# Kernel optimization log

Hardware: AMD Instinct MI355X
Metric: run time of the kernel (lower is better)

## Reference

```python
import jax, jax.numpy as jnp
import numpy as np

N_NODES = 100000
N_EDGES = 1000000
N_GRAPHS = 512
IN_N, IN_E, HID, OUT = 32, 16, 64, 64
EPS = 0.1  # GINEConv eps buffer (not trainable)


def _mlp2(x, w0, b0, w1, b1):
    # 2-layer MLP: Linear -> ReLU -> Linear
    return jax.nn.relu(x @ w0 + b0) @ w1 + b1


def setup_inputs() -> dict:
    key = jax.random.key(0)
    ks = jax.random.split(key, 24)
    s = 0.05
    inp = {
        "x": jax.random.normal(ks[0], (N_NODES, IN_N), jnp.float32),
        "edge_index": jax.random.randint(ks[1], (2, N_EDGES), 0, N_NODES, jnp.int32),
        "edge_attr": jax.random.normal(ks[2], (N_EDGES, IN_E), jnp.float32),
        "batch": jnp.sort(jax.random.randint(ks[3], (N_NODES,), 0, N_GRAPHS, jnp.int32)),
        # node init MLP
        "wn0": jax.random.normal(ks[4], (IN_N, HID)) * s, "bn0": jnp.zeros((HID,)),
        "wn1": jax.random.normal(ks[5], (HID, HID)) * s, "bn1": jnp.zeros((HID,)),
        # edge init MLP
        "we0": jax.random.normal(ks[6], (IN_E, HID)) * s, "be0": jnp.zeros((HID,)),
        "we1": jax.random.normal(ks[7], (HID, HID)) * s, "be1": jnp.zeros((HID,)),
        # 3 residual GINE convs, MLP weights stacked on leading layer axis
        "cw0": jax.random.normal(ks[8], (3, HID, HID)) * s, "cb0": jnp.zeros((3, HID)),
        "cw1": jax.random.normal(ks[9], (3, HID, HID)) * s, "cb1": jnp.zeros((3, HID)),
        # final GINE conv MLP (hidden -> out)
        "lw0": jax.random.normal(ks[10], (HID, HID)) * s, "lb0": jnp.zeros((HID,)),
        "lw1": jax.random.normal(ks[11], (HID, OUT)) * s, "lb1": jnp.zeros((OUT,)),
    }
    return inp


def _gine_conv(x, src, dst, e, w0, b0, w1, b1):
    # message = relu(x_j + edge_attr); aggregate = scatter-add at target i
    msg = jax.nn.relu(x[src] + e)                       # [E, H]
    agg = jax.ops.segment_sum(msg, dst, num_segments=x.shape[0])  # [N, H]
    out = agg + (1.0 + EPS) * x
    return _mlp2(out, w0, b0, w1, b1)


def reference(x, edge_index, edge_attr, batch,
              wn0, bn0, wn1, bn1, we0, be0, we1, be1,
              cw0, cb0, cw1, cb1, lw0, lb0, lw1, lb1):
    src, dst = edge_index[0], edge_index[1]
    h = _mlp2(x, wn0, bn0, wn1, bn1)          # [N, HID]
    e = _mlp2(edge_attr, we0, be0, we1, be1)  # [E, HID]
    for l in range(3):  # residual GINE layers (BatchNorm never applied in source forward)
        h = jax.nn.relu(h + _gine_conv(h, src, dst, e, cw0[l], cb0[l], cw1[l], cb1[l]))
    h = _gine_conv(h, src, dst, e, lw0, lb0, lw1, lb1)  # [N, OUT]
    return jax.ops.segment_sum(h, batch, num_segments=N_GRAPHS)  # global_add_pool -> [G, OUT]
```

## Files before the change

### kernel.cpp

```cpp
#include <hip/hip_runtime.h>
#include <hip/hip_bf16.h>
#include <stdint.h>

#define N_NODES 100000
#define N_EDGES 1000000
#define N_GRAPHS 512
#define HID 64
#define INN 32
#define INE 16
#define CPAD 32

#define NPB 256
#define NBKT ((N_NODES + NPB - 1) / NPB)
#define BCAP 4096

#define S_NW0 0
#define S_NW1 4
#define S_EW0 12
#define S_EW1 16
#define S_CW0 24
#define S_CW1 48
#define S_LW0 72
#define S_LW1 80
#define NSLOT 88

typedef unsigned int uint32;
typedef unsigned short ushort16;
typedef __attribute__((ext_vector_type(8))) short bf8;
typedef __attribute__((ext_vector_type(4))) float f32x4;

__device__ __forceinline__ ushort16 f2bf(float f) {
    uint32 u = __float_as_uint(f);
    uint32 r = (u + 0x7fffu + ((u >> 16) & 1u)) >> 16;
    return (ushort16)r;
}
__device__ __forceinline__ uint32 pack_bf2(float lo, float hi) {
    return (uint32)f2bf(lo) | ((uint32)f2bf(hi) << 16);
}
__device__ __forceinline__ float bf_lo(uint32 v) { return __uint_as_float(v << 16); }
__device__ __forceinline__ float bf_hi(uint32 v) { return __uint_as_float(v & 0xffff0000u); }

__device__ __forceinline__ uint32 pack_h2(float lo, float hi) {
    union { _Float16 h[2]; uint32 u; } cv;
    cv.h[0] = (_Float16)lo; cv.h[1] = (_Float16)hi;
    return cv.u;
}
__device__ __forceinline__ float h2_lo(uint32 v) {
    union { uint32 u; _Float16 h[2]; } cv; cv.u = v; return (float)cv.h[0];
}
__device__ __forceinline__ float h2_hi(uint32 v) {
    union { uint32 u; _Float16 h[2]; } cv; cv.u = v; return (float)cv.h[1];
}
__device__ __forceinline__ uint32 pk_add_f16(uint32 a, uint32 b) {
    uint32 r; asm("v_pk_add_f16 %0, %1, %2" : "=v"(r) : "v"(a), "v"(b)); return r;
}
__device__ __forceinline__ uint32 pk_max_f16(uint32 a, uint32 b) {
    uint32 r; asm("v_pk_max_f16 %0, %1, %2" : "=v"(r) : "v"(a), "v"(b)); return r;
}


__global__ void k_diag(float* out, float val) { out[threadIdx.x] = val; }


__global__ __launch_bounds__(256) void k_prep(
    const float* __restrict__ wn0, const float* __restrict__ wn1,
    const float* __restrict__ we0, const float* __restrict__ we1,
    const float* __restrict__ cw0, const float* __restrict__ cw1,
    const float* __restrict__ lw0, const float* __restrict__ lw1,
    uint32* __restrict__ wfrag)
{
    for (int idx = threadIdx.x; idx < NSLOT * 64; idx += 256) {
        int s = idx >> 6, lane = idx & 63;
        const float* w; int K, NF, base;
        if (s < 4)       { w = wn0; K = 32; NF = 1; base = S_NW0; }
        else if (s < 12) { w = wn1; K = 64; NF = 2; base = S_NW1; }
        else if (s < 16) { w = we0; K = 16; NF = 1; base = S_EW0; }
        else if (s < 24) { w = we1; K = 64; NF = 2; base = S_EW1; }
        else if (s < 48) { int l = (s - S_CW0) >> 3; w = cw0 + l * 4096; K = 64; NF = 2; base = S_CW0 + l * 8; }
        else if (s < 72) { int l = (s - S_CW1) >> 3; w = cw1 + l * 4096; K = 64; NF = 2; base = S_CW1 + l * 8; }
        else if (s < 80) { w = lw0; K = 64; NF = 2; base = S_LW0; }
        else             { w = lw1; K = 64; NF = 2; base = S_LW1; }
        int r = s - base, t = r / NF, f = r - t * NF;
        int quad = lane >> 4, mn = lane & 15;
        uint32 out[4];
        #pragma unroll
        for (int p = 0; p < 4; p++) {
            int k0 = f * 32 + quad * 8 + p * 2;
            float lo = (k0 < K)     ? w[(size_t)k0 * HID + t * 16 + mn]       : 0.f;
            float hi = (k0 + 1 < K) ? w[(size_t)(k0 + 1) * HID + t * 16 + mn] : 0.f;
            out[p] = pack_bf2(lo, hi);
        }
        *(uint4*)(wfrag + (size_t)idx * 4) = make_uint4(out[0], out[1], out[2], out[3]);
    }
}


__global__ __launch_bounds__(256) void k_binA(const int* __restrict__ src,
                                              const int* __restrict__ dst,
                                              int* __restrict__ bcursor,
                                              uint2* __restrict__ binned) {
    __shared__ int cnt[NBKT];
    __shared__ int cur[NBKT];
    const int t = threadIdx.x;
    for (int b = t; b < NBKT; b += 256) cnt[b] = 0;
    __syncthreads();
    const int base = blockIdx.x * 4096;
    #pragma unroll
    for (int j = 0; j < 16; j++) {
        int e = base + j * 256 + t;
        if (e < N_EDGES) atomicAdd(&cnt[dst[e] >> 8], 1);
    }
    __syncthreads();
    for (int b = t; b < NBKT; b += 256) {
        int c = cnt[b];
        cur[b] = (c > 0) ? atomicAdd(&bcursor[(size_t)b * CPAD], c) : 0;
    }
    __syncthreads();
    #pragma unroll
    for (int j = 0; j < 16; j++) {
        int e = base + j * 256 + t;
        if (e < N_EDGES) {
            int d = dst[e];
            int bkt = d >> 8;
            int r = atomicAdd(&cur[bkt], 1);
            if (r < BCAP)
                binned[(size_t)bkt * BCAP + r] =
                    make_uint2((uint32)src[e] | ((uint32)(d & (NPB - 1)) << 17), (uint32)e);
        }
    }
}

__global__ __launch_bounds__(512) void k_scanB(const int* __restrict__ bcursor,
                                               int* __restrict__ bbase) {
    __shared__ int sh[512];
    const int t = threadIdx.x;
    int v = (t < NBKT) ? min(bcursor[(size_t)t * CPAD], BCAP) : 0;
    sh[t] = v; __syncthreads();
    for (int off = 1; off < 512; off <<= 1) {
        int u = (t >= off) ? sh[t - off] : 0;
        __syncthreads();
        sh[t] += u;
        __syncthreads();
    }
    if (t < NBKT) bbase[t] = sh[t] - v;
}

__global__ __launch_bounds__(256) void k_bucketB(const int* __restrict__ bcursor,
                                                 const int* __restrict__ bbase,
                                                 const uint2* __restrict__ binned,
                                                 int* __restrict__ rowptr,
                                                 int* __restrict__ perm_src,
                                                 int* __restrict__ eperm) {
    __shared__ int cnt[NPB];
    __shared__ int sh[NPB];
    const int b = blockIdx.x, t = threadIdx.x;
    const int n = min(bcursor[(size_t)b * CPAD], BCAP);
    const int base = bbase[b];
    const uint2* brec = binned + (size_t)b * BCAP;
    cnt[t] = 0;
    __syncthreads();
    for (int i = t; i < n; i += 256)
        atomicAdd(&cnt[brec[i].x >> 17], 1);
    __syncthreads();
    int c = cnt[t];
    sh[t] = c; __syncthreads();
    for (int off = 1; off < NPB; off <<= 1) {
        int u = (t >= off) ? sh[t - off] : 0;
        __syncthreads();
        sh[t] += u;
        __syncthreads();
    }
    int excl = sh[t] - c;
    int g = b * NPB + t;
    if (g < N_NODES) rowptr[g] = base + excl;
    if (b == 0 && t == 0) rowptr[N_NODES] = N_EDGES;
    cnt[t] = excl;
    __syncthreads();
    for (int i = t; i < n; i += 256) {
        uint2 r = brec[i];
        int dl = (int)(r.x >> 17);
        int p = base + atomicAdd(&cnt[dl], 1);
        perm_src[p] = (int)(r.x & 0x1FFFFu);
        eperm[p] = (int)r.y;
    }
}


template<int NF, bool RELU_RES, bool BF_IN>
__global__ __launch_bounds__(256, 4) void k_mlp_mfma(
    const void* __restrict__ in, const float* __restrict__ hprev, float* __restrict__ out,
    const uint32* __restrict__ wf0, const float* __restrict__ b0,
    const uint32* __restrict__ wf1, const float* __restrict__ b1,
    uint32* __restrict__ out_bf, int nrows)
{
    __shared__ ushort tile[4][16 * 72];
    const int wave = threadIdx.x >> 6, lane = threadIdx.x & 63;
    const int quad = lane >> 4, mn = lane & 15;
    ushort* T = &tile[wave][0];

    bf8 w0f[4][NF];
    #pragma unroll
    for (int t = 0; t < 4; t++)
        #pragma unroll
        for (int f = 0; f < NF; f++)
            w0f[t][f] = *(const bf8*)(wf0 + ((size_t)(t * NF + f) * 64 + lane) * 4);
    bf8 w1f[4][2];
    #pragma unroll
    for (int t = 0; t < 4; t++)
        #pragma unroll
        for (int f = 0; f < 2; f++)
            w1f[t][f] = *(const bf8*)(wf1 + ((size_t)(t * 2 + f) * 64 + lane) * 4);
    float b0v[4], b1v[4];
    #pragma unroll
    for (int t = 0; t < 4; t++) { b0v[t] = b0[t*16+mn]; b1v[t] = b1[t*16+mn]; }

    const int ebase = blockIdx.x * 64 + wave * 16;
    int rowA = ebase + mn; if (rowA > nrows - 1) rowA = nrows - 1;
    bf8 a1[NF];
    if (BF_IN) {
        const ushort* row = (const ushort*)in + (size_t)rowA * HID;
        #pragma unroll
        for (int f = 0; f < NF; f++)
            a1[f] = *(const bf8*)(row + f * 32 + quad * 8);
    } else {
        const float* inf = (const float*)in;
        #pragma unroll
        for (int f = 0; f < NF; f++) {
            const float4* pr = (const float4*)(inf + (size_t)rowA * (NF * 32) + f * 32 + quad * 8);
            float4 v0 = pr[0], v1 = pr[1];
            a1[f][0]=(short)f2bf(v0.x); a1[f][1]=(short)f2bf(v0.y);
            a1[f][2]=(short)f2bf(v0.z); a1[f][3]=(short)f2bf(v0.w);
            a1[f][4]=(short)f2bf(v1.x); a1[f][5]=(short)f2bf(v1.y);
            a1[f][6]=(short)f2bf(v1.z); a1[f][7]=(short)f2bf(v1.w);
        }
    }
    #pragma unroll
    for (int t = 0; t < 4; t++) {
        f32x4 c = {0.f, 0.f, 0.f, 0.f};
        #pragma unroll
        for (int f = 0; f < NF; f++)
            c = __builtin_amdgcn_mfma_f32_16x16x32_bf16(a1[f], w0f[t][f], c, 0, 0, 0);
        #pragma unroll
        for (int rg = 0; rg < 4; rg++) {
            int row = quad * 4 + rg;
            T[row * 72 + t * 16 + mn] = f2bf(fmaxf(c[rg] + b0v[t], 0.f));
        }
    }
    __builtin_amdgcn_wave_barrier();
    bf8 a2[2];
    #pragma unroll
    for (int f = 0; f < 2; f++)
        a2[f] = *(const bf8*)&T[mn * 72 + f * 32 + quad * 8];
    #pragma unroll
    for (int t = 0; t < 4; t++) {
        f32x4 c = {0.f, 0.f, 0.f, 0.f};
        c = __builtin_amdgcn_mfma_f32_16x16x32_bf16(a2[0], w1f[t][0], c, 0, 0, 0);
        c = __builtin_amdgcn_mfma_f32_16x16x32_bf16(a2[1], w1f[t][1], c, 0, 0, 0);
        #pragma unroll
        for (int rg = 0; rg < 4; rg++) {
            int row = quad * 4 + rg;
            int rowg = ebase + row;
            int rowc = (rowg < nrows) ? rowg : (nrows - 1);
            float v = c[rg] + b1v[t];
            if (RELU_RES) {
                float hv = hprev[(size_t)rowc * HID + t * 16 + mn];
                v = fmaxf(v + hv, 0.f);
            }
            if (rowg < nrows) out[(size_t)rowg * HID + t * 16 + mn] = v;
            T[row * 72 + t * 16 + mn] = f2bf(v);
        }
    }
    if (out_bf) {
        __builtin_amdgcn_wave_barrier();
        int half = lane >> 5, c32 = lane & 31;
        #pragma unroll
        for (int rr = 0; rr < 8; rr++) {
            int row = rr * 2 + half;
            int pos = ebase + row;
            if (pos < nrows) {
                uint32 w = *(const uint32*)&T[row * 72 + c32 * 2];
                out_bf[(size_t)pos * 32 + c32] = pack_h2(bf_lo(w), bf_hi(w));
            }
        }
    }
}


__global__ __launch_bounds__(256, 4) void k_edge_mlp_mfma(
    const float* __restrict__ eattr, const int* __restrict__ eperm,
    uint32* __restrict__ e_sorted, const uint32* __restrict__ wfrag,
    const float* __restrict__ b0, const float* __restrict__ b1)
{
    __shared__ ushort tile[4][16 * 72];
    const int wave = threadIdx.x >> 6, lane = threadIdx.x & 63;
    const int quad = lane >> 4, mn = lane & 15;
    ushort* T = &tile[wave][0];

    bf8 w0f[4];
    #pragma unroll
    for (int t = 0; t < 4; t++)
        w0f[t] = *(const bf8*)(wfrag + ((size_t)(S_EW0 + t) * 64 + lane) * 4);
    bf8 w1f[4][2];
    #pragma unroll
    for (int t = 0; t < 4; t++)
        #pragma unroll
        for (int f = 0; f < 2; f++)
            w1f[t][f] = *(const bf8*)(wfrag + ((size_t)(S_EW1 + t * 2 + f) * 64 + lane) * 4);
    float b0v[4], b1v[4];
    #pragma unroll
    for (int t = 0; t < 4; t++) { b0v[t] = b0[t*16+mn]; b1v[t] = b1[t*16+mn]; }

    const int nT = N_EDGES / 16;
    const int stride = gridDim.x * 4;
    int t = blockIdx.x * 4 + wave;

    int ep0 = (t < nT) ? eperm[t * 16 + mn] : 0;
    int ep1 = (t + stride < nT) ? eperm[(t + stride) * 16 + mn] : 0;
    float4 va = make_float4(0.f,0.f,0.f,0.f), vb = va;
    if (quad < 2 && t < nT) {
        const float4* pr = (const float4*)(eattr + (size_t)ep0 * INE + quad * 8);
        va = pr[0]; vb = pr[1];
    }

    for (; t < nT; t += stride) {
        const int tn = t + stride;
        float4 na = make_float4(0.f,0.f,0.f,0.f), nb = na;
        if (quad < 2 && tn < nT) {
            const float4* pr = (const float4*)(eattr + (size_t)ep1 * INE + quad * 8);
            na = pr[0]; nb = pr[1];
        }
        int ep2 = (t + 2 * stride < nT) ? eperm[(t + 2 * stride) * 16 + mn] : 0;

        bf8 a1 = {};
        if (quad < 2) {
            a1[0]=(short)f2bf(va.x); a1[1]=(short)f2bf(va.y);
            a1[2]=(short)f2bf(va.z); a1[3]=(short)f2bf(va.w);
            a1[4]=(short)f2bf(vb.x); a1[5]=(short)f2bf(vb.y);
            a1[6]=(short)f2bf(vb.z); a1[7]=(short)f2bf(vb.w);
        }
        #pragma unroll
        for (int t4 = 0; t4 < 4; t4++) {
            f32x4 c = {0.f, 0.f, 0.f, 0.f};
            c = __builtin_amdgcn_mfma_f32_16x16x32_bf16(a1, w0f[t4], c, 0, 0, 0);
            #pragma unroll
            for (int rg = 0; rg < 4; rg++) {
                int row = quad * 4 + rg;
                T[row * 72 + t4 * 16 + mn] = f2bf(fmaxf(c[rg] + b0v[t4], 0.f));
            }
        }
        __builtin_amdgcn_wave_barrier();
        bf8 a2[2];
        #pragma unroll
        for (int f = 0; f < 2; f++)
            a2[f] = *(const bf8*)&T[mn * 72 + f * 32 + quad * 8];
        #pragma unroll
        for (int t4 = 0; t4 < 4; t4++) {
            f32x4 c = {0.f, 0.f, 0.f, 0.f};
            c = __builtin_amdgcn_mfma_f32_16x16x32_bf16(a2[0], w1f[t4][0], c, 0, 0, 0);
            c = __builtin_amdgcn_mfma_f32_16x16x32_bf16(a2[1], w1f[t4][1], c, 0, 0, 0);
            #pragma unroll
            for (int rg = 0; rg < 4; rg++) {
                int row = quad * 4 + rg;
                T[row * 72 + t4 * 16 + mn] = f2bf(c[rg] + b1v[t4]);
            }
        }
        __builtin_amdgcn_wave_barrier();
        int half = lane >> 5, c32 = lane & 31;
        #pragma unroll
        for (int rr = 0; rr < 8; rr++) {
            int row = rr * 2 + half;
            uint32 w = *(const uint32*)&T[row * 72 + c32 * 2];
            e_sorted[((size_t)t * 16 + row) * 32 + c32] = pack_h2(bf_lo(w), bf_hi(w));
        }
        __builtin_amdgcn_wave_barrier();
        va = na; vb = nb; ep1 = ep2;
    }
}


template<bool RELU_RES, bool BF_OUT>
__global__ __launch_bounds__(256, 4) void k_layer(
    float* __restrict__ h, const uint32* __restrict__ bf_in,
    uint32* __restrict__ bf_out, const uint32* __restrict__ e_sorted,
    const int* __restrict__ rowptr, const int* __restrict__ perm_src,
    const uint32* __restrict__ wf0, const float* __restrict__ b0,
    const uint32* __restrict__ wf1, const float* __restrict__ b1)
{
    __shared__ ushort tile[4][16 * 72];
    const int wave = threadIdx.x >> 6, lane = threadIdx.x & 63;
    const int quad = lane >> 4, mn = lane & 15;
    const int half = lane >> 5, c = lane & 31;
    ushort* T = &tile[wave][0];

    const int nbase = blockIdx.x * 64 + wave * 16;
    const uint32 zero2 = 0u;

    int rp = rowptr[min(nbase + (int)lane, N_NODES)];
    #pragma unroll 1
    for (int i = 0; i < 16; i++) {
        int r0 = __shfl(rp, i), r1 = __shfl(rp, i + 1);
        int nodec = min(nbase + i, N_NODES - 1);
        const float2 hn = *(const float2*)&h[(size_t)nodec * HID + 2 * c];
        uint32 acc = zero2;
        #pragma unroll 1
        for (int base = r0; base < r1; base += 16) {
            int idxs[8]; int sidx[8];
            #pragma unroll
            for (int j = 0; j < 8; j++) {
                int idx = base + 2 * j + half;
                idxs[j] = idx;
                int idxc = (idx < r1) ? idx : (r1 - 1);
                sidx[j] = perm_src[idxc];
            }
            uint32 hv[8], ev[8];
            #pragma unroll
            for (int j = 0; j < 8; j++) {
                int idxc = (idxs[j] < r1) ? idxs[j] : (r1 - 1);
                hv[j] = bf_in[(size_t)sidx[j] * 32 + c];
                ev[j] = e_sorted[(size_t)idxc * 32 + c];
            }
            #pragma unroll
            for (int j = 0; j < 8; j++) {
                uint32 m = pk_max_f16(pk_add_f16(hv[j], ev[j]), zero2);
                m = (idxs[j] < r1) ? m : 0u;
                acc = pk_add_f16(acc, m);
            }
        }
        float accx = h2_lo(acc), accy = h2_hi(acc);
        accx += __shfl_xor(accx, 32);
        accy += __shfl_xor(accy, 32);
        if (half == 0)
            *(uint32*)&T[i * 72 + 2 * c] = pack_bf2(fmaf(1.1f, hn.x, accx),
                                                    fmaf(1.1f, hn.y, accy));
    }
    __builtin_amdgcn_wave_barrier();

    bf8 w0f[4][2], w1f[4][2];
    #pragma unroll
    for (int t = 0; t < 4; t++)
        #pragma unroll
        for (int f = 0; f < 2; f++) {
            w0f[t][f] = *(const bf8*)(wf0 + ((size_t)(t * 2 + f) * 64 + lane) * 4);
            w1f[t][f] = *(const bf8*)(wf1 + ((size_t)(t * 2 + f) * 64 + lane) * 4);
        }
    float b0v[4], b1v[4];
    #pragma unroll
    for (int t = 0; t < 4; t++) { b0v[t] = b0[t*16+mn]; b1v[t] = b1[t*16+mn]; }

    bf8 a1[2];
    #pragma unroll
    for (int f = 0; f < 2; f++)
        a1[f] = *(const bf8*)&T[mn * 72 + f * 32 + quad * 8];
    #pragma unroll
    for (int t = 0; t < 4; t++) {
        f32x4 cc = {0.f, 0.f, 0.f, 0.f};
        cc = __builtin_amdgcn_mfma_f32_16x16x32_bf16(a1[0], w0f[t][0], cc, 0, 0, 0);
        cc = __builtin_amdgcn_mfma_f32_16x16x32_bf16(a1[1], w0f[t][1], cc, 0, 0, 0);
        #pragma unroll
        for (int rg = 0; rg < 4; rg++) {
            int row = quad * 4 + rg;
            T[row * 72 + t * 16 + mn] = f2bf(fmaxf(cc[rg] + b0v[t], 0.f));
        }
    }
    __builtin_amdgcn_wave_barrier();
    bf8 a2[2];
    #pragma unroll
    for (int f = 0; f < 2; f++)
        a2[f] = *(const bf8*)&T[mn * 72 + f * 32 + quad * 8];
    #pragma unroll
    for (int t = 0; t < 4; t++) {
        f32x4 cc = {0.f, 0.f, 0.f, 0.f};
        cc = __builtin_amdgcn_mfma_f32_16x16x32_bf16(a2[0], w1f[t][0], cc, 0, 0, 0);
        cc = __builtin_amdgcn_mfma_f32_16x16x32_bf16(a2[1], w1f[t][1], cc, 0, 0, 0);
        #pragma unroll
        for (int rg = 0; rg < 4; rg++) {
            int row = quad * 4 + rg;
            int rowg = nbase + row;
            int rowc = (rowg < N_NODES) ? rowg : (N_NODES - 1);
            float v = cc[rg] + b1v[t];
            if (RELU_RES) {
                float hv = h[(size_t)rowc * HID + t * 16 + mn];
                v = fmaxf(v + hv, 0.f);
            }
            if (rowg < N_NODES) h[(size_t)rowg * HID + t * 16 + mn] = v;
            T[row * 72 + t * 16 + mn] = f2bf(v);
        }
    }
    if (BF_OUT) {
        __builtin_amdgcn_wave_barrier();
        #pragma unroll
        for (int rr = 0; rr < 8; rr++) {
            int row = rr * 2 + half;
            int pos = nbase + row;
            if (pos < N_NODES) {
                uint32 w = *(const uint32*)&T[row * 72 + c * 2];
                bf_out[(size_t)pos * 32 + c] = pack_h2(bf_lo(w), bf_hi(w));
            }
        }
    }
}


__global__ __launch_bounds__(256) void k_pool(
    const float* __restrict__ h, const int* __restrict__ batch, float* __restrict__ out)
{
    int g = blockIdx.x;
    int lane = threadIdx.x & 63, wave = threadIdx.x >> 6;
    int lo = 0, hi = N_NODES;
    while (lo < hi) { int mid = (lo + hi) >> 1; if (batch[mid] < g) lo = mid + 1; else hi = mid; }
    int start = lo;
    hi = N_NODES;
    while (lo < hi) { int mid = (lo + hi) >> 1; if (batch[mid] < g + 1) lo = mid + 1; else hi = mid; }
    int end = lo;
    float acc = 0.f;
    for (int n = start + wave; n < end; n += 4)
        acc += h[(size_t)n*HID + lane];
    __shared__ float sh[4][64];
    sh[wave][lane] = acc;
    __syncthreads();
    if (wave == 0)
        out[(size_t)g*HID + lane] = sh[0][lane] + sh[1][lane] + sh[2][lane] + sh[3][lane];
}


extern "C" void kernel_launch(void* const* d_in, const int* in_sizes, int n_in,
                              void* d_out, int out_size, void* d_ws, size_t ws_size,
                              hipStream_t stream) {
    const float* x     = (const float*)d_in[0];
    const int*   eidx  = (const int*)  d_in[1];
    const float* eattr = (const float*)d_in[2];
    const int*   batch = (const int*)  d_in[3];
    const float* wn0 = (const float*)d_in[4];  const float* bn0 = (const float*)d_in[5];
    const float* wn1 = (const float*)d_in[6];  const float* bn1 = (const float*)d_in[7];
    const float* we0 = (const float*)d_in[8];  const float* be0 = (const float*)d_in[9];
    const float* we1 = (const float*)d_in[10]; const float* be1 = (const float*)d_in[11];
    const float* cw0 = (const float*)d_in[12]; const float* cb0 = (const float*)d_in[13];
    const float* cw1 = (const float*)d_in[14]; const float* cb1 = (const float*)d_in[15];
    const float* lw0 = (const float*)d_in[16]; const float* lb0 = (const float*)d_in[17];
    const float* lw1 = (const float*)d_in[18]; const float* lb1 = (const float*)d_in[19];
    const int* src = eidx;
    const int* dst = eidx + N_EDGES;

    char* ws = (char*)d_ws;
    size_t off = 0;
    auto alloc = [&](size_t bytes) -> void* {
        void* p = ws + off;
        off = (off + bytes + 255) & ~(size_t)255;
        return p;
    };
    int*    bcursor  = (int*)  alloc((size_t)NBKT * CPAD * 4);
    int*    bbase    = (int*)  alloc((size_t)NBKT * 4);
    uint2*  binned   = (uint2*)alloc((size_t)NBKT * BCAP * 8);
    int*    rowptr   = (int*)  alloc((size_t)(N_NODES + 1) * 4);
    int*    perm_src = (int*)  alloc((size_t)N_EDGES * 4);
    int*    eperm    = (int*)  alloc((size_t)N_EDGES * 4);
    float*  h        = (float*)alloc((size_t)N_NODES * HID * 4);
    uint32* bfB      = (uint32*)alloc((size_t)N_NODES * 32 * 4);
    uint32* bfA      = (uint32*)alloc((size_t)N_NODES * 32 * 4);
    uint32* e_sorted = (uint32*)alloc((size_t)N_EDGES * HID * 2);
    uint32* wfrag    = (uint32*)alloc((size_t)NSLOT * 64 * 16);
    if (off > ws_size) {
        k_diag<<<1, 64, 0, stream>>>((float*)d_out, 1.0e9f);
        return;
    }

    k_prep<<<1, 256, 0, stream>>>(wn0, wn1, we0, we1, cw0, cw1, lw0, lw1, wfrag);

    hipMemsetAsync(bcursor, 0, (size_t)NBKT * CPAD * 4, stream);
    k_binA<<<(N_EDGES + 4095) / 4096, 256, 0, stream>>>(src, dst, bcursor, binned);
    k_scanB<<<1, 512, 0, stream>>>(bcursor, bbase);
    k_bucketB<<<NBKT, 256, 0, stream>>>(bcursor, bbase, binned, rowptr, perm_src, eperm);

    const int MGRID = (N_NODES + 63) / 64;

    k_mlp_mfma<1, false, false><<<MGRID, 256, 0, stream>>>(
        x, nullptr, h, wfrag + S_NW0 * 256, bn0, wfrag + S_NW1 * 256, bn1, bfA, N_NODES);

    k_edge_mlp_mfma<<<2048, 256, 0, stream>>>(eattr, eperm, e_sorted, wfrag, be0, be1);

    k_layer<true, true><<<MGRID, 256, 0, stream>>>(
        h, bfA, bfB, e_sorted, rowptr, perm_src,
        wfrag + (S_CW0 + 0 * 8) * 256, cb0 + 0 * 64, wfrag + (S_CW1 + 0 * 8) * 256, cb1 + 0 * 64);
    k_layer<true, true><<<MGRID, 256, 0, stream>>>(
        h, bfB, bfA, e_sorted, rowptr, perm_src,
        wfrag + (S_CW0 + 1 * 8) * 256, cb0 + 1 * 64, wfrag + (S_CW1 + 1 * 8) * 256, cb1 + 1 * 64);
    k_layer<true, true><<<MGRID, 256, 0, stream>>>(
        h, bfA, bfB, e_sorted, rowptr, perm_src,
        wfrag + (S_CW0 + 2 * 8) * 256, cb0 + 2 * 64, wfrag + (S_CW1 + 2 * 8) * 256, cb1 + 2 * 64);
    k_layer<false, false><<<MGRID, 256, 0, stream>>>(
        h, bfB, bfA, e_sorted, rowptr, perm_src,
        wfrag + S_LW0 * 256, lb0, wfrag + S_LW1 * 256, lb1);

    k_pool<<<N_GRAPHS, 256, 0, stream>>>(h, batch, (float*)d_out);
}
```

Before: 501.7 us.

## Fuse preprocessing kernels, drop scan kernel, stage perm_src in LDS, simplify f16 packing

Merges weight prep with edge binning and bucket sort with the node init MLP into two combined launches. The separate scan kernel is removed by having each bucket block sum preceding bucket counts itself. The layer kernel caches each wave's perm_src slice in LDS and prefetches the next node's h row. MLP outputs are now stored directly as fp16 rather than going bf16 to fp16. Together these cut launch count, serialization and redundant global loads, at the cost of O(NBKT) redundant reads per bucket block.

```diff
diff --git a/kernel.cpp b/kernel.cpp
--- a/kernel.cpp
+++ b/kernel.cpp
@@ -13,6 +13,8 @@
 #define NPB 256
 #define NBKT ((N_NODES + NPB - 1) / NPB)
 #define BCAP 4096
+#define NBB  ((N_EDGES + 4095) / 4096)
+#define PMCAP 320
 
 #define S_NW0 0
 #define S_NW1 4
@@ -40,10 +42,8 @@
 __device__ __forceinline__ float bf_lo(uint32 v) { return __uint_as_float(v << 16); }
 __device__ __forceinline__ float bf_hi(uint32 v) { return __uint_as_float(v & 0xffff0000u); }
 
-__device__ __forceinline__ uint32 pack_h2(float lo, float hi) {
-    union { _Float16 h[2]; uint32 u; } cv;
-    cv.h[0] = (_Float16)lo; cv.h[1] = (_Float16)hi;
-    return cv.u;
+__device__ __forceinline__ unsigned short f2h_u(float f) {
+    union { _Float16 h; unsigned short u; } cv; cv.h = (_Float16)f; return cv.u;
 }
 __device__ __forceinline__ float h2_lo(uint32 v) {
     union { uint32 u; _Float16 h[2]; } cv; cv.u = v; return (float)cv.h[0];
@@ -62,7 +62,7 @@
 __global__ void k_diag(float* out, float val) { out[threadIdx.x] = val; }
 
 
-__global__ __launch_bounds__(256) void k_prep(
+__device__ void dev_prep(
     const float* __restrict__ wn0, const float* __restrict__ wn1,
     const float* __restrict__ we0, const float* __restrict__ we1,
     const float* __restrict__ cw0, const float* __restrict__ cw1,
@@ -94,26 +94,23 @@
     }
 }
 
-
-__global__ __launch_bounds__(256) void k_binA(const int* __restrict__ src,
-                                              const int* __restrict__ dst,
-                                              int* __restrict__ bcursor,
-                                              uint2* __restrict__ binned) {
-    __shared__ int cnt[NBKT];
-    __shared__ int cur[NBKT];
+__device__ void dev_binA(int* cnt, int* cur, int b,
+                         const int* __restrict__ src, const int* __restrict__ dst,
+                         int* __restrict__ bcursor, uint2* __restrict__ binned)
+{
     const int t = threadIdx.x;
-    for (int b = t; b < NBKT; b += 256) cnt[b] = 0;
-    __syncthreads();
-    const int base = blockIdx.x * 4096;
+    for (int k = t; k < NBKT; k += 256) cnt[k] = 0;
+    __syncthreads();
+    const int base = b * 4096;
     #pragma unroll
     for (int j = 0; j < 16; j++) {
         int e = base + j * 256 + t;
         if (e < N_EDGES) atomicAdd(&cnt[dst[e] >> 8], 1);
     }
     __syncthreads();
-    for (int b = t; b < NBKT; b += 256) {
-        int c = cnt[b];
-        cur[b] = (c > 0) ? atomicAdd(&bcursor[(size_t)b * CPAD], c) : 0;
+    for (int k = t; k < NBKT; k += 256) {
+        int c = cnt[k];
+        cur[k] = (c > 0) ? atomicAdd(&bcursor[(size_t)k * CPAD], c) : 0;
     }
     __syncthreads();
     #pragma unroll
@@ -130,47 +127,53 @@
     }
 }
 
-__global__ __launch_bounds__(512) void k_scanB(const int* __restrict__ bcursor,
-                                               int* __restrict__ bbase) {
-    __shared__ int sh[512];
+__global__ __launch_bounds__(256) void k_prep_binA(
+    const int* __restrict__ src, const int* __restrict__ dst,
+    int* __restrict__ bcursor, uint2* __restrict__ binned,
+    const float* __restrict__ wn0, const float* __restrict__ wn1,
+    const float* __restrict__ we0, const float* __restrict__ we1,
+    const float* __restrict__ cw0, const float* __restrict__ cw1,
+    const float* __restrict__ lw0, const float* __restrict__ lw1,
+    uint32* __restrict__ wfrag)
+{
+    __shared__ int cnt[NBKT];
+    __shared__ int cur[NBKT];
+    if (blockIdx.x < NBB) dev_binA(cnt, cur, blockIdx.x, src, dst, bcursor, binned);
+    else                  dev_prep(wn0, wn1, we0, we1, cw0, cw1, lw0, lw1, wfrag);
+}
+
+
+__device__ void dev_bucketB(int* cnt, int* shv, int b,
+                            const int* __restrict__ bcursor, const uint2* __restrict__ binned,
+                            int* __restrict__ rowptr, int* __restrict__ perm_src,
+                            int* __restrict__ eperm)
+{
     const int t = threadIdx.x;
-    int v = (t < NBKT) ? min(bcursor[(size_t)t * CPAD], BCAP) : 0;
-    sh[t] = v; __syncthreads();
-    for (int off = 1; off < 512; off <<= 1) {
-        int u = (t >= off) ? sh[t - off] : 0;
+    int s = 0;
+    for (int k = t; k < b; k += 256) s += min(bcursor[(size_t)k * CPAD], BCAP);
+    shv[t] = s; __syncthreads();
+    for (int off = 128; off > 0; off >>= 1) {
+        if (t < off) shv[t] += shv[t + off];
         __syncthreads();
-        sh[t] += u;
-        __syncthreads();
-    }
-    if (t < NBKT) bbase[t] = sh[t] - v;
-}
-
-__global__ __launch_bounds__(256) void k_bucketB(const int* __restrict__ bcursor,
-                                                 const int* __restrict__ bbase,
-                                                 const uint2* __restrict__ binned,
-                                                 int* __restrict__ rowptr,
-                                                 int* __restrict__ perm_src,
-                                                 int* __restrict__ eperm) {
-    __shared__ int cnt[NPB];
-    __shared__ int sh[NPB];
-    const int b = blockIdx.x, t = threadIdx.x;
+    }
+    const int base = shv[0];
     const int n = min(bcursor[(size_t)b * CPAD], BCAP);
-    const int base = bbase[b];
     const uint2* brec = binned + (size_t)b * BCAP;
+    __syncthreads();
     cnt[t] = 0;
     __syncthreads();
     for (int i = t; i < n; i += 256)
         atomicAdd(&cnt[brec[i].x >> 17], 1);
     __syncthreads();
     int c = cnt[t];
-    sh[t] = c; __syncthreads();
+    shv[t] = c; __syncthreads();
     for (int off = 1; off < NPB; off <<= 1) {
-        int u = (t >= off) ? sh[t - off] : 0;
+        int u = (t >= off) ? shv[t - off] : 0;
         __syncthreads();
-        sh[t] += u;
+        shv[t] += u;
         __syncthreads();
     }
-    int excl = sh[t] - c;
+    int excl = shv[t] - c;
     int g = b * NPB + t;
     if (g < N_NODES) rowptr[g] = base + excl;
     if (b == 0 && t == 0) rowptr[N_NODES] = N_EDGES;
@@ -185,25 +188,19 @@
     }
 }
 
-
-template<int NF, bool RELU_RES, bool BF_IN>
-__global__ __launch_bounds__(256, 4) void k_mlp_mfma(
-    const void* __restrict__ in, const float* __restrict__ hprev, float* __restrict__ out,
-    const uint32* __restrict__ wf0, const float* __restrict__ b0,
-    const uint32* __restrict__ wf1, const float* __restrict__ b1,
-    uint32* __restrict__ out_bf, int nrows)
-{
-    __shared__ ushort tile[4][16 * 72];
-    const int wave = threadIdx.x >> 6, lane = threadIdx.x & 63;
+__device__ void dev_node_mlp(ushort* T, int blk,
+                             const float* __restrict__ x, float* __restrict__ h,
+                             const uint32* __restrict__ wf0, const float* __restrict__ b0,
+                             const uint32* __restrict__ wf1, const float* __restrict__ b1,
+                             uint32* __restrict__ out_bf)
+{
+    const int lane = threadIdx.x & 63;
     const int quad = lane >> 4, mn = lane & 15;
-    ushort* T = &tile[wave][0];
-
-    bf8 w0f[4][NF];
+
+    bf8 w0f[4];
     #pragma unroll
     for (int t = 0; t < 4; t++)
-        #pragma unroll
-        for (int f = 0; f < NF; f++)
-            w0f[t][f] = *(const bf8*)(wf0 + ((size_t)(t * NF + f) * 64 + lane) * 4);
+        w0f[t] = *(const bf8*)(wf0 + ((size_t)t * 64 + lane) * 4);
     bf8 w1f[4][2];
     #pragma unroll
     for (int t = 0; t < 4; t++)
@@ -214,32 +211,21 @@
     #pragma unroll
     for (int t = 0; t < 4; t++) { b0v[t] = b0[t*16+mn]; b1v[t] = b1[t*16+mn]; }
 
-    const int ebase = blockIdx.x * 64 + wave * 16;
-    int rowA = ebase + mn; if (rowA > nrows - 1) rowA = nrows - 1;
-    bf8 a1[NF];
-    if (BF_IN) {
-        const ushort* row = (const ushort*)in + (size_t)rowA * HID;
-        #pragma unroll
-        for (int f = 0; f < NF; f++)
-            a1[f] = *(const bf8*)(row + f * 32 + quad * 8);
-    } else {
-        const float* inf = (const float*)in;
-        #pragma unroll
-        for (int f = 0; f < NF; f++) {
-            const float4* pr = (const float4*)(inf + (size_t)rowA * (NF * 32) + f * 32 + quad * 8);
-            float4 v0 = pr[0], v1 = pr[1];
-            a1[f][0]=(short)f2bf(v0.x); a1[f][1]=(short)f2bf(v0.y);
-            a1[f][2]=(short)f2bf(v0.z); a1[f][3]=(short)f2bf(v0.w);
-            a1[f][4]=(short)f2bf(v1.x); a1[f][5]=(short)f2bf(v1.y);
-            a1[f][6]=(short)f2bf(v1.z); a1[f][7]=(short)f2bf(v1.w);
-        }
+    const int ebase = blk * 64 + (int)(threadIdx.x >> 6) * 16;
+    int rowA = min(ebase + mn, N_NODES - 1);
+    bf8 a1;
+    {
+        const float4* pr = (const float4*)(x + (size_t)rowA * INN + quad * 8);
+        float4 v0 = pr[0], v1 = pr[1];
+        a1[0]=(short)f2bf(v0.x); a1[1]=(short)f2bf(v0.y);
+        a1[2]=(short)f2bf(v0.z); a1[3]=(short)f2bf(v0.w);
+        a1[4]=(short)f2bf(v1.x); a1[5]=(short)f2bf(v1.y);
+        a1[6]=(short)f2bf(v1.z); a1[7]=(short)f2bf(v1.w);
     }
     #pragma unroll
     for (int t = 0; t < 4; t++) {
         f32x4 c = {0.f, 0.f, 0.f, 0.f};
-        #pragma unroll
-        for (int f = 0; f < NF; f++)
-            c = __builtin_amdgcn_mfma_f32_16x16x32_bf16(a1[f], w0f[t][f], c, 0, 0, 0);
+        c = __builtin_amdgcn_mfma_f32_16x16x32_bf16(a1, w0f[t], c, 0, 0, 0);
         #pragma unroll
         for (int rg = 0; rg < 4; rg++) {
             int row = quad * 4 + rg;
@@ -260,29 +246,38 @@
         for (int rg = 0; rg < 4; rg++) {
             int row = quad * 4 + rg;
             int rowg = ebase + row;
-            int rowc = (rowg < nrows) ? rowg : (nrows - 1);
             float v = c[rg] + b1v[t];
-            if (RELU_RES) {
-                float hv = hprev[(size_t)rowc * HID + t * 16 + mn];
-                v = fmaxf(v + hv, 0.f);
-            }
-            if (rowg < nrows) out[(size_t)rowg * HID + t * 16 + mn] = v;
-            T[row * 72 + t * 16 + mn] = f2bf(v);
-        }
-    }
-    if (out_bf) {
-        __builtin_amdgcn_wave_barrier();
-        int half = lane >> 5, c32 = lane & 31;
-        #pragma unroll
-        for (int rr = 0; rr < 8; rr++) {
-            int row = rr * 2 + half;
-            int pos = ebase + row;
-            if (pos < nrows) {
-                uint32 w = *(const uint32*)&T[row * 72 + c32 * 2];
-                out_bf[(size_t)pos * 32 + c32] = pack_h2(bf_lo(w), bf_hi(w));
-            }
-        }
-    }
+            if (rowg < N_NODES) h[(size_t)rowg * HID + t * 16 + mn] = v;
+            T[row * 72 + t * 16 + mn] = f2h_u(v);
+        }
+    }
+    __builtin_amdgcn_wave_barrier();
+    int half = lane >> 5, c32 = lane & 31;
+    #pragma unroll
+    for (int rr = 0; rr < 8; rr++) {
+        int row = rr * 2 + half;
+        int pos = ebase + row;
+        if (pos < N_NODES)
+            out_bf[(size_t)pos * 32 + c32] = *(const uint32*)&T[row * 72 + c32 * 2];
+    }
+}
+
+__global__ __launch_bounds__(256, 4) void k_build_mlp(
+    const int* __restrict__ bcursor, const uint2* __restrict__ binned,
+    int* __restrict__ rowptr, int* __restrict__ perm_src, int* __restrict__ eperm,
+    const float* __restrict__ x, float* __restrict__ h,
+    const uint32* __restrict__ wfrag,
+    const float* __restrict__ bn0, const float* __restrict__ bn1,
+    uint32* __restrict__ out_bf)
+{
+    __shared__ int cnt[NPB];
+    __shared__ int shv[NPB];
+    __shared__ ushort tile[4][16 * 72];
+    if (blockIdx.x < NBKT)
+        dev_bucketB(cnt, shv, blockIdx.x, bcursor, binned, rowptr, perm_src, eperm);
+    else
+        dev_node_mlp(&tile[threadIdx.x >> 6][0], blockIdx.x - NBKT, x, h,
+                     wfrag + S_NW0 * 256, bn0, wfrag + S_NW1 * 256, bn1, out_bf);
 }
 
 
@@ -361,7 +356,7 @@
             #pragma unroll
             for (int rg = 0; rg < 4; rg++) {
                 int row = quad * 4 + rg;
-                T[row * 72 + t4 * 16 + mn] = f2bf(c[rg] + b1v[t4]);
+                T[row * 72 + t4 * 16 + mn] = f2h_u(c[rg] + b1v[t4]);
             }
         }
         __builtin_amdgcn_wave_barrier();
@@ -369,8 +364,7 @@
         #pragma unroll
         for (int rr = 0; rr < 8; rr++) {
             int row = rr * 2 + half;
-            uint32 w = *(const uint32*)&T[row * 72 + c32 * 2];
-            e_sorted[((size_t)t * 16 + row) * 32 + c32] = pack_h2(bf_lo(w), bf_hi(w));
+            e_sorted[((size_t)t * 16 + row) * 32 + c32] = *(const uint32*)&T[row * 72 + c32 * 2];
         }
         __builtin_amdgcn_wave_barrier();
         va = na; vb = nb; ep1 = ep2;
@@ -387,41 +381,51 @@
     const uint32* __restrict__ wf1, const float* __restrict__ b1)
 {
     __shared__ ushort tile[4][16 * 72];
+    __shared__ int pm[4][PMCAP];
     const int wave = threadIdx.x >> 6, lane = threadIdx.x & 63;
     const int quad = lane >> 4, mn = lane & 15;
     const int half = lane >> 5, c = lane & 31;
     ushort* T = &tile[wave][0];
 
     const int nbase = blockIdx.x * 64 + wave * 16;
-    const uint32 zero2 = 0u;
 
     int rp = rowptr[min(nbase + (int)lane, N_NODES)];
+    const int R0w = __shfl(rp, 0), R1w = __shfl(rp, 16);
+    const bool fit = (R1w - R0w) <= PMCAP;
+    if (fit)
+        for (int k = lane; k < R1w - R0w; k += 64) pm[wave][k] = perm_src[R0w + k];
+
+    float2 hn_cur = *(const float2*)&h[(size_t)min(nbase, N_NODES - 1) * HID + 2 * c];
     #pragma unroll 1
     for (int i = 0; i < 16; i++) {
         int r0 = __shfl(rp, i), r1 = __shfl(rp, i + 1);
-        int nodec = min(nbase + i, N_NODES - 1);
-        const float2 hn = *(const float2*)&h[(size_t)nodec * HID + 2 * c];
-        uint32 acc = zero2;
+        float2 hn_nxt = *(const float2*)&h[(size_t)min(nbase + i + 1, N_NODES - 1) * HID + 2 * c];
+        uint32 acc = 0u;
         #pragma unroll 1
         for (int base = r0; base < r1; base += 16) {
-            int idxs[8]; int sidx[8];
+            int idxs[8], idxc[8], sidx[8];
             #pragma unroll
             for (int j = 0; j < 8; j++) {
                 int idx = base + 2 * j + half;
                 idxs[j] = idx;
-                int idxc = (idx < r1) ? idx : (r1 - 1);
-                sidx[j] = perm_src[idxc];
+                idxc[j] = (idx < r1) ? idx : (r1 - 1);
+            }
+            if (fit) {
+                #pragma unroll
+                for (int j = 0; j < 8; j++) sidx[j] = pm[wave][idxc[j] - R0w];
+            } else {
+                #pragma unroll
+                for (int j = 0; j < 8; j++) sidx[j] = perm_src[idxc[j]];
             }
             uint32 hv[8], ev[8];
             #pragma unroll
             for (int j = 0; j < 8; j++) {
-                int idxc = (idxs[j] < r1) ? idxs[j] : (r1 - 1);
                 hv[j] = bf_in[(size_t)sidx[j] * 32 + c];
-                ev[j] = e_sorted[(size_t)idxc * 32 + c];
+                ev[j] = e_sorted[(size_t)idxc[j] * 32 + c];
             }
             #pragma unroll
             for (int j = 0; j < 8; j++) {
-                uint32 m = pk_max_f16(pk_add_f16(hv[j], ev[j]), zero2);
+                uint32 m = pk_max_f16(pk_add_f16(hv[j], ev[j]), 0u);
                 m = (idxs[j] < r1) ? m : 0u;
                 acc = pk_add_f16(acc, m);
             }
@@ -430,8 +434,9 @@
         accx += __shfl_xor(accx, 32);
         accy += __shfl_xor(accy, 32);
         if (half == 0)
-            *(uint32*)&T[i * 72 + 2 * c] = pack_bf2(fmaf(1.1f, hn.x, accx),
-                                                    fmaf(1.1f, hn.y, accy));
+            *(uint32*)&T[i * 72 + 2 * c] = pack_bf2(fmaf(1.1f, hn_cur.x, accx),
+                                                    fmaf(1.1f, hn_cur.y, accy));
+        hn_cur = hn_nxt;
     }
     __builtin_amdgcn_wave_barrier();
 
@@ -483,7 +488,7 @@
                 v = fmaxf(v + hv, 0.f);
             }
             if (rowg < N_NODES) h[(size_t)rowg * HID + t * 16 + mn] = v;
-            T[row * 72 + t * 16 + mn] = f2bf(v);
+            T[row * 72 + t * 16 + mn] = f2h_u(v);
         }
     }
     if (BF_OUT) {
@@ -492,10 +497,8 @@
         for (int rr = 0; rr < 8; rr++) {
             int row = rr * 2 + half;
             int pos = nbase + row;
-            if (pos < N_NODES) {
-                uint32 w = *(const uint32*)&T[row * 72 + c * 2];
-                bf_out[(size_t)pos * 32 + c] = pack_h2(bf_lo(w), bf_hi(w));
-            }
+            if (pos < N_NODES)
+                bf_out[(size_t)pos * 32 + c] = *(const uint32*)&T[row * 72 + c * 2];
         }
     }
 }
@@ -549,7 +552,6 @@
         return p;
     };
     int*    bcursor  = (int*)  alloc((size_t)NBKT * CPAD * 4);
-    int*    bbase    = (int*)  alloc((size_t)NBKT * 4);
     uint2*  binned   = (uint2*)alloc((size_t)NBKT * BCAP * 8);
     int*    rowptr   = (int*)  alloc((size_t)(N_NODES + 1) * 4);
     int*    perm_src = (int*)  alloc((size_t)N_EDGES * 4);
@@ -564,18 +566,13 @@
         return;
     }
 
-    k_prep<<<1, 256, 0, stream>>>(wn0, wn1, we0, we1, cw0, cw1, lw0, lw1, wfrag);
+    const int MGRID = (N_NODES + 63) / 64;
 
     hipMemsetAsync(bcursor, 0, (size_t)NBKT * CPAD * 4, stream);
-    k_binA<<<(N_EDGES + 4095) / 4096, 256, 0, stream>>>(src, dst, bcursor, binned);
-    k_scanB<<<1, 512, 0, stream>>>(bcursor, bbase);
-    k_bucketB<<<NBKT, 256, 0, stream>>>(bcursor, bbase, binned, rowptr, perm_src, eperm);
-
-    const int MGRID = (N_NODES + 63) / 64;
-
-    k_mlp_mfma<1, false, false><<<MGRID, 256, 0, stream>>>(
-        x, nullptr, h, wfrag + S_NW0 * 256, bn0, wfrag + S_NW1 * 256, bn1, bfA, N_NODES);
-
+    k_prep_binA<<<NBB + 1, 256, 0, stream>>>(src, dst, bcursor, binned,
+                                             wn0, wn1, we0, we1, cw0, cw1, lw0, lw1, wfrag);
+    k_build_mlp<<<NBKT + MGRID, 256, 0, stream>>>(bcursor, binned, rowptr, perm_src, eperm,
+                                                  x, h, wfrag, bn0, bn1, bfA);
     k_edge_mlp_mfma<<<2048, 256, 0, stream>>>(eattr, eperm, e_sorted, wfrag, be0, be1);
 
     k_layer<true, true><<<MGRID, 256, 0, stream>>>(
```

New measurement: 459.6 us. 8.4% less time.
